# Kernel tuning notes

Measured on AMD Instinct MI355X. Metric: run time of the kernel, lower is better.

Reference implementation:

```python
import jax, jax.numpy as jnp
import numpy as np

K = 16      # number of soft nearest neighbors
TEMP = 0.1  # softmax temperature


def setup_inputs() -> dict:
    key = jax.random.key(0)
    k1, k2, k3 = jax.random.split(key, 3)
    B, D, N, F = 8, 128, 100000, 128
    return {
        "query": jax.random.normal(k1, (B, D), dtype=jnp.float32),
        "keys": jax.random.normal(k2, (B, D, N), dtype=jnp.float32),
        "values": jax.random.normal(k3, (B, F, N), dtype=jnp.float32),
    }


def reference(query, keys, values):
    # similarity: note the NEGATIVE sign in the original module
    d = query.shape[-1]
    sims = -jnp.einsum('bd,bdn->bn', query, keys) / jnp.asarray(d, query.dtype) ** 0.5  # [B,N]

    alpha0 = jax.nn.softmax(sims, axis=-1)  # [B,N]

    def step(alpha, _):
        w = jax.nn.softmax(alpha / TEMP, axis=-1)      # omega_i, [B,N]
        return alpha + jnp.log1p(-w), w                # alpha += log(1 - omega_i)

    _, ws = jax.lax.scan(step, alpha0, None, length=K)  # ws: [K,B,N]

    # einsum(omega, values, '*B N K, *B F N -> *B K F')
    return jnp.einsum('kbn,bfn->bkf', ws, values)  # [B,K,F]
```

## Files before the change

kernel.cpp:

```cpp
#include <hip/hip_runtime.h>
#include <hip/hip_bf16.h>

#define N_TOK 100000
#define K_ITER 16

typedef __attribute__((ext_vector_type(8))) short short8;
typedef __attribute__((ext_vector_type(4))) float floatx4;

static __device__ __forceinline__ unsigned short f2bf(float x) {
  unsigned u = __float_as_uint(x);
  u += 0x7FFFu + ((u >> 16) & 1u);
  return (unsigned short)(u >> 16);
}

__global__ __launch_bounds__(256) void k_sims(const float* __restrict__ q,
                                              const float* __restrict__ keys,
                                              float* __restrict__ sims,
                                              float* __restrict__ scal) {
  __shared__ float qs[128];
  __shared__ float red[4];
  const int b = blockIdx.y;
  const int tid = threadIdx.x;
  if (tid < 128) qs[tid] = q[b * 128 + tid];
  __syncthreads();
  const int n0 = blockIdx.x * 1024 + tid * 4;
  float part = 0.f;
  if (n0 < N_TOK) {
    const float* kb = keys + (size_t)b * 128 * N_TOK + n0;
    float ax = 0.f, ay = 0.f, az = 0.f, aw = 0.f;
#pragma unroll 8
    for (int d = 0; d < 128; ++d) {
      float4 kv = *(const float4*)(kb + (size_t)d * N_TOK);
      float qd = qs[d];
      ax = fmaf(qd, kv.x, ax); ay = fmaf(qd, kv.y, ay);
      az = fmaf(qd, kv.z, az); aw = fmaf(qd, kv.w, aw);
    }
    const float sc = -0.08838834764831843f;
    float4 s4; s4.x = ax * sc; s4.y = ay * sc; s4.z = az * sc; s4.w = aw * sc;
    *(float4*)(sims + (size_t)b * N_TOK + n0) = s4;
    part = __expf(s4.x) + __expf(s4.y) + __expf(s4.z) + __expf(s4.w);
  }
#pragma unroll
  for (int off = 32; off > 0; off >>= 1) part += __shfl_down(part, off);
  if ((tid & 63) == 0) red[tid >> 6] = part;
  __syncthreads();
  if (tid == 0) atomicAdd(&scal[b * 32], red[0] + red[1] + red[2] + red[3]);
}

__global__ __launch_bounds__(256) void k_mom(const float* __restrict__ sims,
                                             float* __restrict__ scal) {
  __shared__ float red[3][4];
  const int b = blockIdx.y;
  const int tid = threadIdx.x;
  const float r0 = 1.f / scal[b * 32];
  const int n0 = blockIdx.x * 1024 + tid * 4;
  float m1 = 0.f, m2 = 0.f, m3 = 0.f;
  if (n0 < N_TOK) {
    float4 s4 = *(const float4*)(sims + (size_t)b * N_TOK + n0);
    float e;
    e = __expf(10.f * __expf(s4.x) * r0); m1 += e; m2 += e * e; m3 += e * e * e;
    e = __expf(10.f * __expf(s4.y) * r0); m1 += e; m2 += e * e; m3 += e * e * e;
    e = __expf(10.f * __expf(s4.z) * r0); m1 += e; m2 += e * e; m3 += e * e * e;
    e = __expf(10.f * __expf(s4.w) * r0); m1 += e; m2 += e * e; m3 += e * e * e;
  }
#pragma unroll
  for (int off = 32; off > 0; off >>= 1) {
    m1 += __shfl_down(m1, off); m2 += __shfl_down(m2, off); m3 += __shfl_down(m3, off);
  }
  if ((tid & 63) == 0) { int w = tid >> 6; red[0][w] = m1; red[1][w] = m2; red[2][w] = m3; }
  __syncthreads();
  if (tid == 0) {
    atomicAdd(&scal[b * 32 + 1], red[0][0] + red[0][1] + red[0][2] + red[0][3]);
    atomicAdd(&scal[b * 32 + 2], red[1][0] + red[1][1] + red[1][2] + red[1][3]);
    atomicAdd(&scal[b * 32 + 3], red[2][0] + red[2][1] + red[2][2] + red[2][3]);
  }
}

__global__ __launch_bounds__(256) void k_main(const float* __restrict__ sims,
                                              const float* __restrict__ values,
                                              const float* __restrict__ scal,
                                              float* __restrict__ outacc) {
  __shared__ unsigned short Vlds[128][136];
  __shared__ unsigned short Wlds[16][136];
  const int b = blockIdx.y;
  const int tid = threadIdx.x;
  const float r0 = 1.f / scal[b * 32 + 0];
  float S  = scal[b * 32 + 1];
  float m2 = scal[b * 32 + 2];
  float m3 = scal[b * 32 + 3];
  float R[K_ITER];
#pragma unroll
  for (int k = 0; k < K_ITER; ++k) {
    float r = 1.f / S;
    R[k] = r;
    S  = S - 10.f * r * m2 + 45.f * r * r * m3;
    m2 = m2 - 20.f * r * m3;
  }
  const float* vb = values + (size_t)b * 128 * N_TOK;
  const int lane = tid & 63, wv = tid >> 6;
  const int col = lane & 15, quad = lane >> 4;
  floatx4 acc0 = {0.f, 0.f, 0.f, 0.f};
  floatx4 acc1 = {0.f, 0.f, 0.f, 0.f};

  for (int c = blockIdx.x; c < 782; c += 112) {
    const int nb = c * 128;
    __syncthreads();
#pragma unroll
    for (int i = 0; i < 16; ++i) {
      int L = tid + i * 256;
      int f = L >> 5, jj = L & 31;
      int n = nb + jj * 4;
      uint2 pk; pk.x = 0u; pk.y = 0u;
      if (n < N_TOK) {
        float4 v = *(const float4*)(vb + (size_t)f * N_TOK + n);
        pk.x = (unsigned)f2bf(v.x) | ((unsigned)f2bf(v.y) << 16);
        pk.y = (unsigned)f2bf(v.z) | ((unsigned)f2bf(v.w) << 16);
      }
      *(uint2*)&Vlds[f][jj * 4] = pk;
    }
    if (tid < 128) {
      int n = nb + tid;
      bool valid = n < N_TOK;
      float E = 0.f;
      if (valid) {
        float s0 = sims[(size_t)b * N_TOK + n];
        E = __expf(10.f * __expf(s0) * r0);
      }
#pragma unroll
      for (int k = 0; k < K_ITER; ++k) {
        unsigned short wb = 0;
        if (valid) {
          float w = E * R[k];
          wb = f2bf(w);
          E *= fmaf(w, fmaf(45.f, w, -10.f), 1.f);
        }
        Wlds[k][tid] = wb;
      }
    }
    __syncthreads();
#pragma unroll
    for (int s = 0; s < 4; ++s) {
      int no = s * 32 + quad * 8;
      short8 af = *(const short8*)&Wlds[col][no];
      short8 b0 = *(const short8*)&Vlds[wv * 32 + col][no];
      short8 b1 = *(const short8*)&Vlds[wv * 32 + 16 + col][no];
      acc0 = __builtin_amdgcn_mfma_f32_16x16x32_bf16(af, b0, acc0, 0, 0, 0);
      acc1 = __builtin_amdgcn_mfma_f32_16x16x32_bf16(af, b1, acc1, 0, 0, 0);
    }
  }
#pragma unroll
  for (int r = 0; r < 4; ++r) {
    int ko = quad * 4 + r;
    atomicAdd(&outacc[((b << 4) + ko) * 128 + wv * 32 + col], acc0[r]);
    atomicAdd(&outacc[((b << 4) + ko) * 128 + wv * 32 + 16 + col], acc1[r]);
  }
}

__global__ __launch_bounds__(256) void k_out(const float* __restrict__ outacc,
                                             float* __restrict__ out) {
  int i = blockIdx.x * 256 + threadIdx.x;
  if (i < 16384) out[i] = outacc[i];
}

extern "C" void kernel_launch(void* const* d_in, const int* in_sizes, int n_in,
                              void* d_out, int out_size, void* d_ws, size_t ws_size,
                              hipStream_t stream) {
  const float* q      = (const float*)d_in[0];
  const float* keys   = (const float*)d_in[1];
  const float* values = (const float*)d_in[2];
  float* outacc = (float*)d_ws;
  float* scal   = outacc + 16384;
  float* sims   = scal + 256;
  hipMemsetAsync(d_ws, 0, (16384 + 256) * sizeof(float), stream);
  dim3 g1(98, 8);
  k_sims<<<g1, 256, 0, stream>>>(q, keys, sims, scal);
  k_mom<<<g1, 256, 0, stream>>>(sims, scal);
  dim3 g3(112, 8);
  k_main<<<g3, 256, 0, stream>>>(sims, values, scal, outacc);
  k_out<<<64, 256, 0, stream>>>(outacc, (float*)d_out);
}
```

Measured before the change: 770.7 us.

## Load values directly into MFMA B fragments, double-buffer weight tile

The main kernel no longer stages the values tile through shared memory. Each lane loads its own float4 pairs from global memory, converts them to bf16 and feeds them straight into the MFMA B operand. The chunk size grows to 256 tokens, the softmax-weight tile is double-buffered so only one barrier per chunk is needed, and the next chunk's sims value is prefetched. This removes the LDS write/read traffic and one barrier per chunk. In exchange, the per-lane global loads are 32-byte strided-row reads that may coalesce less well, and the grid is reduced to 98 blocks in x.

```diff
diff --git a/kernel.cpp b/kernel.cpp
--- a/kernel.cpp
+++ b/kernel.cpp
@@ -3,6 +3,9 @@
 
 #define N_TOK 100000
 #define K_ITER 16
+#define CHUNK 256
+#define NCHUNK 391
+#define GX 98
 
 typedef __attribute__((ext_vector_type(8))) short short8;
 typedef __attribute__((ext_vector_type(4))) float floatx4;
@@ -11,6 +14,15 @@
   unsigned u = __float_as_uint(x);
   u += 0x7FFFu + ((u >> 16) & 1u);
   return (unsigned short)(u >> 16);
+}
+
+static __device__ __forceinline__ short8 pack8(float4 a, float4 b) {
+  union { unsigned u[4]; short8 s; } r;
+  r.u[0] = (unsigned)f2bf(a.x) | ((unsigned)f2bf(a.y) << 16);
+  r.u[1] = (unsigned)f2bf(a.z) | ((unsigned)f2bf(a.w) << 16);
+  r.u[2] = (unsigned)f2bf(b.x) | ((unsigned)f2bf(b.y) << 16);
+  r.u[3] = (unsigned)f2bf(b.z) | ((unsigned)f2bf(b.w) << 16);
+  return r.s;
 }
 
 __global__ __launch_bounds__(256) void k_sims(const float* __restrict__ q,
@@ -80,8 +92,7 @@
                                               const float* __restrict__ values,
                                               const float* __restrict__ scal,
                                               float* __restrict__ outacc) {
-  __shared__ unsigned short Vlds[128][136];
-  __shared__ unsigned short Wlds[16][136];
+  __shared__ __align__(16) unsigned short Wlds[2][16][264];
   const int b = blockIdx.y;
   const int tid = threadIdx.x;
   const float r0 = 1.f / scal[b * 32 + 0];
@@ -96,57 +107,57 @@
     S  = S - 10.f * r * m2 + 45.f * r * r * m3;
     m2 = m2 - 20.f * r * m3;
   }
-  const float* vb = values + (size_t)b * 128 * N_TOK;
   const int lane = tid & 63, wv = tid >> 6;
   const int col = lane & 15, quad = lane >> 4;
+  const float* rowA = values + (size_t)b * 128 * N_TOK + (size_t)(wv * 32 + col) * N_TOK;
+  const float* rowB = rowA + (size_t)16 * N_TOK;
+  const float* simb = sims + (size_t)b * N_TOK;
   floatx4 acc0 = {0.f, 0.f, 0.f, 0.f};
   floatx4 acc1 = {0.f, 0.f, 0.f, 0.f};
 
-  for (int c = blockIdx.x; c < 782; c += 112) {
-    const int nb = c * 128;
-    __syncthreads();
-#pragma unroll
-    for (int i = 0; i < 16; ++i) {
-      int L = tid + i * 256;
-      int f = L >> 5, jj = L & 31;
-      int n = nb + jj * 4;
-      uint2 pk; pk.x = 0u; pk.y = 0u;
-      if (n < N_TOK) {
-        float4 v = *(const float4*)(vb + (size_t)f * N_TOK + n);
-        pk.x = (unsigned)f2bf(v.x) | ((unsigned)f2bf(v.y) << 16);
-        pk.y = (unsigned)f2bf(v.z) | ((unsigned)f2bf(v.w) << 16);
-      }
-      *(uint2*)&Vlds[f][jj * 4] = pk;
-    }
-    if (tid < 128) {
-      int n = nb + tid;
-      bool valid = n < N_TOK;
-      float E = 0.f;
-      if (valid) {
-        float s0 = sims[(size_t)b * N_TOK + n];
-        E = __expf(10.f * __expf(s0) * r0);
-      }
+  int c = blockIdx.x;
+  int np = c * CHUNK + tid;
+  float sv = (np < N_TOK) ? simb[np] : 0.f;
+  int p = 0;
+  for (; c < NCHUNK; c += GX) {
+    const int nb = c * CHUNK;
+    {
+      const bool valid = (nb + tid) < N_TOK;
+      float E = valid ? __expf(10.f * __expf(sv) * r0) : 0.f;
 #pragma unroll
       for (int k = 0; k < K_ITER; ++k) {
-        unsigned short wb = 0;
-        if (valid) {
-          float w = E * R[k];
-          wb = f2bf(w);
-          E *= fmaf(w, fmaf(45.f, w, -10.f), 1.f);
-        }
-        Wlds[k][tid] = wb;
+        float w = E * R[k];
+        Wlds[p][k][tid] = f2bf(w);
+        E *= fmaf(w, fmaf(45.f, w, -10.f), 1.f);
       }
     }
+    {
+      int cn = c + GX;
+      np = cn * CHUNK + tid;
+      sv = (cn < NCHUNK && np < N_TOK) ? simb[np] : 0.f;
+    }
     __syncthreads();
-#pragma unroll
-    for (int s = 0; s < 4; ++s) {
-      int no = s * 32 + quad * 8;
-      short8 af = *(const short8*)&Wlds[col][no];
-      short8 b0 = *(const short8*)&Vlds[wv * 32 + col][no];
-      short8 b1 = *(const short8*)&Vlds[wv * 32 + 16 + col][no];
+#pragma unroll 4
+    for (int sb = 0; sb < 8; ++sb) {
+      const int no = sb * 32 + quad * 8;
+      const int n = nb + no;
+      short8 af = *(const short8*)&Wlds[p][col][no];
+      short8 b0, b1;
+      if (n < N_TOK) {
+        float4 a0 = *(const float4*)(rowA + n);
+        float4 a1 = *(const float4*)(rowA + n + 4);
+        float4 c0 = *(const float4*)(rowB + n);
+        float4 c1 = *(const float4*)(rowB + n + 4);
+        b0 = pack8(a0, a1);
+        b1 = pack8(c0, c1);
+      } else {
+        b0 = (short8)0;
+        b1 = (short8)0;
+      }
       acc0 = __builtin_amdgcn_mfma_f32_16x16x32_bf16(af, b0, acc0, 0, 0, 0);
       acc1 = __builtin_amdgcn_mfma_f32_16x16x32_bf16(af, b1, acc1, 0, 0, 0);
     }
+    p ^= 1;
   }
 #pragma unroll
   for (int r = 0; r < 4; ++r) {
@@ -175,7 +186,7 @@
   dim3 g1(98, 8);
   k_sims<<<g1, 256, 0, stream>>>(q, keys, sims, scal);
   k_mom<<<g1, 256, 0, stream>>>(sims, scal);
-  dim3 g3(112, 8);
+  dim3 g3(GX, 8);
   k_main<<<g3, 256, 0, stream>>>(sims, values, scal, outacc);
   k_out<<<64, 256, 0, stream>>>(outacc, (float*)d_out);
 }
```

New measurement: 773.8 us. Within noise of the previous version (+0.4%).
